# Optimization experiments

Measured on AMD Instinct MI355X. Metric: run time of the kernel, lower is better.

The kernel has to match this reference:

```python
import jax, jax.numpy as jnp
import numpy as np

NF, NLOC, NALL, NNEI = 2, 2048, 3072, 128
Q_DIM = K_DIM = V_DIM = 256
H, D = 8, 32  # num_heads, head_dim
TOTAL = H * D


def setup_inputs() -> dict:
    key = jax.random.key(0)
    ks = jax.random.split(key, 12)
    inp = {
        "q": jax.random.normal(ks[0], (NF, NLOC, Q_DIM), jnp.float32),
        "k": jax.random.normal(ks[1], (NF, NALL, K_DIM), jnp.float32),
        "v": jax.random.normal(ks[2], (NF, NALL, V_DIM), jnp.float32),
        "nlist": jax.random.randint(ks[3], (NF, NLOC, NNEI), 0, NALL, jnp.int64),
        "bias": jax.random.normal(ks[4], (NF, H, NLOC, NNEI), jnp.float32),
        # torch Linear weights: [out, in]
        "Wq": jax.random.normal(ks[5], (TOTAL, Q_DIM), jnp.float32) * 0.05,
        "Wk": jax.random.normal(ks[6], (TOTAL, K_DIM), jnp.float32) * 0.05,
        "Wv": jax.random.normal(ks[7], (TOTAL, V_DIM), jnp.float32) * 0.05,
        "Wg": jax.random.normal(ks[8], (TOTAL, Q_DIM), jnp.float32) * 0.05,
        "bg": jnp.ones((TOTAL,), jnp.float32),  # gating init: bias=1
        "Wo": jax.random.normal(ks[9], (Q_DIM, TOTAL), jnp.float32) * 0.05,
        "bo": jnp.zeros((Q_DIM,), jnp.float32),
    }
    return inp


def reference(q, k, v, nlist, bias, Wq, Wk, Wv, Wg, bg, Wo, bo):
    nf, nloc, _ = q.shape
    nnei = nlist.shape[-1]
    norm = D ** (-0.5)

    g = q @ Wg.T + bg                       # [nf, nloc, TOTAL]
    qh = (q @ Wq.T) * norm                  # [nf, nloc, TOTAL]
    kh = k @ Wk.T                           # [nf, nall, TOTAL]
    vh = v @ Wv.T                           # [nf, nall, TOTAL]

    # gather neighbors: [nf, nloc, nnei, TOTAL]
    fidx = jnp.arange(nf)[:, None, None]
    kg = kh[fidx, nlist].reshape(nf, nloc, nnei, H, D)
    vg = vh[fidx, nlist].reshape(nf, nloc, nnei, H, D)
    qh = qh.reshape(nf, nloc, H, D)

    # per-atom attention: single query vs nnei neighbors
    attn = jnp.einsum("fnhd,fnihd->fhni", qh, kg)      # [nf, H, nloc, nnei]
    attn = jax.nn.softmax(attn + bias, axis=-1)
    o = jnp.einsum("fhni,fnihd->fnhd", attn, vg)       # [nf, nloc, H, D]
    o = o.reshape(nf, nloc, TOTAL)

    o = jax.nn.sigmoid(g) * o
    return o @ Wo.T + bo
```

## Files before the change

kernel.cpp:

```cpp
#include <hip/hip_runtime.h>

#define NF_   2
#define NLOC_ 2048
#define NALL_ 3072
#define NNEI_ 128
#define H_    8
#define D_    32
#define CH_   256

typedef __attribute__((ext_vector_type(8))) short  short8v;
typedef __attribute__((ext_vector_type(8))) unsigned short ushort8v;
typedef __attribute__((ext_vector_type(4))) float  floatx4;

__device__ __forceinline__ unsigned short f2bf(float x) {
  unsigned u = __float_as_uint(x);
  unsigned r = u + 0x7fff + ((u >> 16) & 1);
  return (unsigned short)(r >> 16);
}
__device__ __forceinline__ float bf2f(unsigned short h) {
  return __uint_as_float(((unsigned)h) << 16);
}

__device__ __forceinline__ void cvt_store(unsigned short* hp, unsigned short* lp,
                                          float4 u, float4 v) {
  ushort8v hv, lv;
  hv[0] = f2bf(u.x); lv[0] = f2bf(u.x - bf2f(hv[0]));
  hv[1] = f2bf(u.y); lv[1] = f2bf(u.y - bf2f(hv[1]));
  hv[2] = f2bf(u.z); lv[2] = f2bf(u.z - bf2f(hv[2]));
  hv[3] = f2bf(u.w); lv[3] = f2bf(u.w - bf2f(hv[3]));
  hv[4] = f2bf(v.x); lv[4] = f2bf(v.x - bf2f(hv[4]));
  hv[5] = f2bf(v.y); lv[5] = f2bf(v.y - bf2f(hv[5]));
  hv[6] = f2bf(v.z); lv[6] = f2bf(v.z - bf2f(hv[6]));
  hv[7] = f2bf(v.w); lv[7] = f2bf(v.w - bf2f(hv[7]));
  *(ushort8v*)hp = hv;
  *(ushort8v*)lp = lv;
}

__global__ __launch_bounds__(256) void wcvt_kernel(
    const float* __restrict__ W0, const float* __restrict__ W1,
    const float* __restrict__ W2, const float* __restrict__ W3,
    const float* __restrict__ W4, unsigned short* __restrict__ dst) {
  const float* srcs[5] = {W0, W1, W2, W3, W4};
  const float* s = srcs[blockIdx.y];
  unsigned short* hi = dst + (size_t)blockIdx.y * 2 * 65536;
  unsigned short* lo = hi + 65536;
  const int idx = (blockIdx.x * 256 + threadIdx.x) * 4;
  const float4 v = *(const float4*)(s + idx);
  unsigned short h0 = f2bf(v.x), h1 = f2bf(v.y), h2 = f2bf(v.z), h3 = f2bf(v.w);
  ushort4 hv = {h0, h1, h2, h3};
  ushort4 lv = {f2bf(v.x - bf2f(h0)), f2bf(v.y - bf2f(h1)),
                f2bf(v.z - bf2f(h2)), f2bf(v.w - bf2f(h3))};
  *(ushort4*)(hi + idx) = hv;
  *(ushort4*)(lo + idx) = lv;
}

__device__ __forceinline__ void gemm_mfma(
    const float* __restrict__ A,
    const unsigned short* __restrict__ Whi, const unsigned short* __restrict__ Wlo,
    const float* __restrict__ bvec, float* __restrict__ C,
    int M, int mode,
    unsigned short (*Ah)[40], unsigned short (*Al)[40],
    unsigned short (*Wh)[40], unsigned short (*Wl)[40]) {
  const int t  = threadIdx.x;
  const int m0 = blockIdx.y * 128;
  if (m0 >= M) return;
  const int n0 = blockIdx.x * 64;

  const int lane = t & 63;
  const int wv   = t >> 6;
  const int wr   = wv >> 1;
  const int wc   = wv & 1;
  const int l15  = lane & 15;
  const int ko   = (lane >> 4) * 8;

  const int sr = t >> 1;
  const int sk = (t & 1) * 16;
  const int wrow = t >> 2;
  const int wk   = (t & 3) * 8;

  floatx4 acc[4][2] = {};

  for (int k0 = 0; k0 < 256; k0 += 32) {
    const float* Ap = A + (size_t)(m0 + sr) * 256 + k0 + sk;
    const float4 a0 = *(const float4*)(Ap + 0);
    const float4 a1 = *(const float4*)(Ap + 4);
    const float4 a2 = *(const float4*)(Ap + 8);
    const float4 a3 = *(const float4*)(Ap + 12);
    const size_t woff = (size_t)(n0 + wrow) * 256 + k0 + wk;
    const uint4 whv = *(const uint4*)(Whi + woff);
    const uint4 wlv = *(const uint4*)(Wlo + woff);
    __syncthreads();
    cvt_store(&Ah[sr][sk + 0], &Al[sr][sk + 0], a0, a1);
    cvt_store(&Ah[sr][sk + 8], &Al[sr][sk + 8], a2, a3);
    *(uint4*)&Wh[wrow][wk] = whv;
    *(uint4*)&Wl[wrow][wk] = wlv;
    __syncthreads();

    short8v afh[4], afl[4], bfh[2], bfl[2];
#pragma unroll
    for (int mi = 0; mi < 4; ++mi) {
      const int rr = wr * 64 + mi * 16 + l15;
      afh[mi] = *(const short8v*)&Ah[rr][ko];
      afl[mi] = *(const short8v*)&Al[rr][ko];
    }
#pragma unroll
    for (int ni = 0; ni < 2; ++ni) {
      const int rr = wc * 32 + ni * 16 + l15;
      bfh[ni] = *(const short8v*)&Wh[rr][ko];
      bfl[ni] = *(const short8v*)&Wl[rr][ko];
    }
#pragma unroll
    for (int mi = 0; mi < 4; ++mi)
#pragma unroll
      for (int ni = 0; ni < 2; ++ni) {
        acc[mi][ni] = __builtin_amdgcn_mfma_f32_16x16x32_bf16(
            afh[mi], bfh[ni], acc[mi][ni], 0, 0, 0);
        acc[mi][ni] = __builtin_amdgcn_mfma_f32_16x16x32_bf16(
            afh[mi], bfl[ni], acc[mi][ni], 0, 0, 0);
        acc[mi][ni] = __builtin_amdgcn_mfma_f32_16x16x32_bf16(
            afl[mi], bfh[ni], acc[mi][ni], 0, 0, 0);
      }
  }

  const float norm = 0.17677669529663687f;
#pragma unroll
  for (int mi = 0; mi < 4; ++mi)
#pragma unroll
    for (int ni = 0; ni < 2; ++ni) {
      const int col = n0 + wc * 32 + ni * 16 + l15;
      const float bv = (mode == 1 || mode == 3) ? bvec[col] : 0.f;
#pragma unroll
      for (int r = 0; r < 4; ++r) {
        const int row = m0 + wr * 64 + mi * 16 + (lane >> 4) * 4 + r;
        float vv = acc[mi][ni][r];
        if (mode == 0)      vv *= norm;
        else if (mode == 1) vv = 1.f / (1.f + __expf(-(vv + bv)));
        else if (mode == 3) vv += bv;
        C[(size_t)row * 256 + col] = vv;
      }
    }
}

__global__ __launch_bounds__(256, 3) void proj_kernel(
    const float* __restrict__ q, const float* __restrict__ k, const float* __restrict__ v,
    const unsigned short* __restrict__ whl, const float* __restrict__ bg,
    float* __restrict__ qh, float* __restrict__ gs,
    float* __restrict__ kh, float* __restrict__ vh) {
  __shared__ unsigned short Ah[128][40], Al[128][40], Wh[64][40], Wl[64][40];
  const unsigned short* Whi = whl + (size_t)blockIdx.z * 2 * 65536;
  const unsigned short* Wlo = Whi + 65536;
  switch (blockIdx.z) {
    case 0:  gemm_mfma(q, Whi, Wlo, nullptr, qh, NF_ * NLOC_, 0, Ah, Al, Wh, Wl); break;
    case 1:  gemm_mfma(q, Whi, Wlo, bg,      gs, NF_ * NLOC_, 1, Ah, Al, Wh, Wl); break;
    case 2:  gemm_mfma(k, Whi, Wlo, nullptr, kh, NF_ * NALL_, 2, Ah, Al, Wh, Wl); break;
    default: gemm_mfma(v, Whi, Wlo, nullptr, vh, NF_ * NALL_, 2, Ah, Al, Wh, Wl); break;
  }
}

__global__ __launch_bounds__(256, 3) void out_gemm_kernel(
    const float* __restrict__ x, const unsigned short* __restrict__ whl,
    const float* __restrict__ bo, float* __restrict__ out) {
  __shared__ unsigned short Ah[128][40], Al[128][40], Wh[64][40], Wl[64][40];
  const unsigned short* Whi = whl + (size_t)4 * 2 * 65536;
  const unsigned short* Wlo = Whi + 65536;
  gemm_mfma(x, Whi, Wlo, bo, out, NF_ * NLOC_, 3, Ah, Al, Wh, Wl);
}

__global__ __launch_bounds__(256, 4) void attn_kernel(
    const float* __restrict__ qh, const float* __restrict__ gs,
    const float* __restrict__ kh, const float* __restrict__ vh,
    const void* __restrict__ nlist, const float* __restrict__ bias,
    float* __restrict__ x) {
  __shared__ float q_s[CH_];
  __shared__ int   jn[NNEI_];
  __shared__ float p[H_][NNEI_ + 4];
  __shared__ float K_s[32][256];

  const int t   = threadIdx.x;
  const int bid = blockIdx.x;
  const int f   = bid >> 11;
  const int n   = bid & (NLOC_ - 1);
  const size_t row = (size_t)bid;

  q_s[t] = qh[row * CH_ + t];

  const int* nl32 = (const int*)nlist;
  int odd_or = 0;
#pragma unroll
  for (int w = 1; w < 16; w += 2) odd_or |= nl32[w];
  if (t < NNEI_) {
    if (odd_or == 0) {
      const long long* nl64 = (const long long*)nlist;
      jn[t] = (int)nl64[row * NNEI_ + t];
    } else {
      jn[t] = nl32[row * NNEI_ + t];
    }
  }
  __syncthreads();

  const int h  = t >> 5;
  const int il = t & 31;
  const int w  = t >> 6;
  const int l  = t & 63;

  float4 qv[8];
  {
    const float4* qp = (const float4*)(q_s + h * D_);
#pragma unroll
    for (int i = 0; i < 8; ++i) qv[i] = qp[i];
  }

  const float* kbase = kh + (size_t)f * NALL_ * CH_;
  const float* bb    = bias + (((size_t)f * H_ + h) * NLOC_ + n) * NNEI_;

  float s[4];
#pragma unroll
  for (int c = 0; c < 4; ++c) {
    if (c) __syncthreads();
#pragma unroll
    for (int u = 0; u < 8; ++u) {
      const int r = w * 8 + u;
      const int j = jn[c * 32 + r];
      const float4 kv = *(const float4*)(kbase + (size_t)j * CH_ + l * 4);
      *(float4*)(&K_s[r][(l ^ (r & 7)) * 4]) = kv;
    }
    __syncthreads();
    const int swz = il & 7;
    const float4* krow = (const float4*)(&K_s[il][0]);
    float a = 0.f;
#pragma unroll
    for (int d4 = 0; d4 < 8; ++d4) {
      const float4 kv = krow[(h * 8 + d4) ^ swz];
      a = fmaf(qv[d4].x, kv.x, a);
      a = fmaf(qv[d4].y, kv.y, a);
      a = fmaf(qv[d4].z, kv.z, a);
      a = fmaf(qv[d4].w, kv.w, a);
    }
    s[c] = a + bb[c * 32 + il];
  }

  float m = fmaxf(fmaxf(s[0], s[1]), fmaxf(s[2], s[3]));
#pragma unroll
  for (int off = 16; off >= 1; off >>= 1) m = fmaxf(m, __shfl_xor(m, off));
  float e[4];
  float sum = 0.f;
#pragma unroll
  for (int r = 0; r < 4; ++r) { e[r] = __expf(s[r] - m); sum += e[r]; }
#pragma unroll
  for (int off = 16; off >= 1; off >>= 1) sum += __shfl_xor(sum, off);
  const float inv = 1.f / sum;
#pragma unroll
  for (int r = 0; r < 4; ++r) p[h][il + 32 * r] = e[r] * inv;
  __syncthreads();

  const float* vb = vh + (size_t)f * NALL_ * CH_ + h * D_ + il;
  float ac0 = 0.f, ac1 = 0.f, ac2 = 0.f, ac3 = 0.f;
  for (int i = 0; i < NNEI_; i += 4) {
    const float4 p4 = *(const float4*)(&p[h][i]);
    const int4  j4 = *(const int4*)(&jn[i]);
    ac0 = fmaf(p4.x, vb[(size_t)j4.x * CH_], ac0);
    ac1 = fmaf(p4.y, vb[(size_t)j4.y * CH_], ac1);
    ac2 = fmaf(p4.z, vb[(size_t)j4.z * CH_], ac2);
    ac3 = fmaf(p4.w, vb[(size_t)j4.w * CH_], ac3);
  }
  const float acc = (ac0 + ac1) + (ac2 + ac3);

  const float g = gs[row * CH_ + t];
  x[row * CH_ + t] = g * acc;
}

extern "C" void kernel_launch(void* const* d_in, const int* in_sizes, int n_in,
                              void* d_out, int out_size, void* d_ws, size_t ws_size,
                              hipStream_t stream) {
  const float* q     = (const float*)d_in[0];
  const float* k     = (const float*)d_in[1];
  const float* v     = (const float*)d_in[2];
  const void*  nlist = d_in[3];
  const float* bias  = (const float*)d_in[4];
  const float* Wq    = (const float*)d_in[5];
  const float* Wk    = (const float*)d_in[6];
  const float* Wv    = (const float*)d_in[7];
  const float* Wg    = (const float*)d_in[8];
  const float* bg    = (const float*)d_in[9];
  const float* Wo    = (const float*)d_in[10];
  const float* bo    = (const float*)d_in[11];
  float* out = (float*)d_out;

  float* ws = (float*)d_ws;
  float* qh = ws;
  float* gs = qh + (size_t)NF_ * NLOC_ * CH_;
  float* kh = gs + (size_t)NF_ * NLOC_ * CH_;
  float* vh = kh + (size_t)NF_ * NALL_ * CH_;
  float* x  = vh + (size_t)NF_ * NALL_ * CH_;
  unsigned short* whl = (unsigned short*)(x + (size_t)NF_ * NLOC_ * CH_);

  wcvt_kernel<<<dim3(64, 5), 256, 0, stream>>>(Wq, Wg, Wk, Wv, Wo, whl);
  proj_kernel<<<dim3(4, 48, 4), 256, 0, stream>>>(q, k, v, whl, bg,
                                                  qh, gs, kh, vh);
  attn_kernel<<<dim3(NF_ * NLOC_), 256, 0, stream>>>(qh, gs, kh, vh, nlist, bias, x);
  out_gemm_kernel<<<dim3(4, 32), 256, 0, stream>>>(x, whl, bo, out);
}
```

Measured before the change: 185.3 us.

## Pre-split activations to bf16 hi/lo and vectorize attention PV gather

Adds a separate conversion pass that splits q/k/v into bf16 hi/lo arrays once, so the projection GEMM tiles only copy pre-split data instead of converting fp32 in every block (q was converted twice, once for the Wq and once for the Wg projection). The attention kernel now writes its output directly as bf16 hi/lo, which removes the conversion from the output GEMM. The PV accumulation is restructured so each wave takes a quarter of the neighbors and loads float4 vectors of V, with a cross-wave reduction in shared memory. The cost is an extra kernel launch and extra global traffic for the hi/lo activation copies.

```diff
diff --git a/kernel.cpp b/kernel.cpp
--- a/kernel.cpp
+++ b/kernel.cpp
@@ -19,21 +19,6 @@
 }
 __device__ __forceinline__ float bf2f(unsigned short h) {
   return __uint_as_float(((unsigned)h) << 16);
-}
-
-__device__ __forceinline__ void cvt_store(unsigned short* hp, unsigned short* lp,
-                                          float4 u, float4 v) {
-  ushort8v hv, lv;
-  hv[0] = f2bf(u.x); lv[0] = f2bf(u.x - bf2f(hv[0]));
-  hv[1] = f2bf(u.y); lv[1] = f2bf(u.y - bf2f(hv[1]));
-  hv[2] = f2bf(u.z); lv[2] = f2bf(u.z - bf2f(hv[2]));
-  hv[3] = f2bf(u.w); lv[3] = f2bf(u.w - bf2f(hv[3]));
-  hv[4] = f2bf(v.x); lv[4] = f2bf(v.x - bf2f(hv[4]));
-  hv[5] = f2bf(v.y); lv[5] = f2bf(v.y - bf2f(hv[5]));
-  hv[6] = f2bf(v.z); lv[6] = f2bf(v.z - bf2f(hv[6]));
-  hv[7] = f2bf(v.w); lv[7] = f2bf(v.w - bf2f(hv[7]));
-  *(ushort8v*)hp = hv;
-  *(ushort8v*)lp = lv;
 }
 
 __global__ __launch_bounds__(256) void wcvt_kernel(
@@ -54,8 +39,33 @@
   *(ushort4*)(lo + idx) = lv;
 }
 
+#define QN_ ((size_t)NF_ * NLOC_ * CH_)
+#define KN_ ((size_t)NF_ * NALL_ * CH_)
+
+__global__ __launch_bounds__(256) void acvt_kernel(
+    const float* __restrict__ q, const float* __restrict__ k,
+    const float* __restrict__ v, unsigned short* __restrict__ dst) {
+  const int m = blockIdx.y;
+  const float* src;
+  unsigned short* hi;
+  size_t n;
+  if (m == 0)      { src = q; hi = dst;                 n = QN_; }
+  else if (m == 1) { src = k; hi = dst + 2 * QN_;       n = KN_; }
+  else             { src = v; hi = dst + 2 * QN_ + 2 * KN_; n = KN_; }
+  unsigned short* lo = hi + n;
+  const size_t idx = ((size_t)blockIdx.x * 256 + threadIdx.x) * 4;
+  if (idx >= n) return;
+  const float4 val = *(const float4*)(src + idx);
+  unsigned short h0 = f2bf(val.x), h1 = f2bf(val.y), h2 = f2bf(val.z), h3 = f2bf(val.w);
+  ushort4 hv = {h0, h1, h2, h3};
+  ushort4 lv = {f2bf(val.x - bf2f(h0)), f2bf(val.y - bf2f(h1)),
+                f2bf(val.z - bf2f(h2)), f2bf(val.w - bf2f(h3))};
+  *(ushort4*)(hi + idx) = hv;
+  *(ushort4*)(lo + idx) = lv;
+}
+
 __device__ __forceinline__ void gemm_mfma(
-    const float* __restrict__ A,
+    const unsigned short* __restrict__ Ahi, const unsigned short* __restrict__ Alo,
     const unsigned short* __restrict__ Whi, const unsigned short* __restrict__ Wlo,
     const float* __restrict__ bvec, float* __restrict__ C,
     int M, int mode,
@@ -81,19 +91,22 @@
   floatx4 acc[4][2] = {};
 
   for (int k0 = 0; k0 < 256; k0 += 32) {
-    const float* Ap = A + (size_t)(m0 + sr) * 256 + k0 + sk;
-    const float4 a0 = *(const float4*)(Ap + 0);
-    const float4 a1 = *(const float4*)(Ap + 4);
-    const float4 a2 = *(const float4*)(Ap + 8);
-    const float4 a3 = *(const float4*)(Ap + 12);
+    const unsigned short* Aph = Ahi + (size_t)(m0 + sr) * 256 + k0 + sk;
+    const unsigned short* Apl = Alo + (size_t)(m0 + sr) * 256 + k0 + sk;
+    const ushort8v ah0 = *(const ushort8v*)(Aph);
+    const ushort8v ah1 = *(const ushort8v*)(Aph + 8);
+    const ushort8v al0 = *(const ushort8v*)(Apl);
+    const ushort8v al1 = *(const ushort8v*)(Apl + 8);
     const size_t woff = (size_t)(n0 + wrow) * 256 + k0 + wk;
-    const uint4 whv = *(const uint4*)(Whi + woff);
-    const uint4 wlv = *(const uint4*)(Wlo + woff);
+    const ushort8v whv = *(const ushort8v*)(Whi + woff);
+    const ushort8v wlv = *(const ushort8v*)(Wlo + woff);
     __syncthreads();
-    cvt_store(&Ah[sr][sk + 0], &Al[sr][sk + 0], a0, a1);
-    cvt_store(&Ah[sr][sk + 8], &Al[sr][sk + 8], a2, a3);
-    *(uint4*)&Wh[wrow][wk] = whv;
-    *(uint4*)&Wl[wrow][wk] = wlv;
+    *(ushort8v*)&Ah[sr][sk + 0] = ah0;
+    *(ushort8v*)&Ah[sr][sk + 8] = ah1;
+    *(ushort8v*)&Al[sr][sk + 0] = al0;
+    *(ushort8v*)&Al[sr][sk + 8] = al1;
+    *(ushort8v*)&Wh[wrow][wk] = whv;
+    *(ushort8v*)&Wl[wrow][wk] = wlv;
     __syncthreads();
 
     short8v afh[4], afl[4], bfh[2], bfl[2];
@@ -142,35 +155,38 @@
 }
 
 __global__ __launch_bounds__(256, 3) void proj_kernel(
-    const float* __restrict__ q, const float* __restrict__ k, const float* __restrict__ v,
-    const unsigned short* __restrict__ whl, const float* __restrict__ bg,
+    const unsigned short* __restrict__ ahl, const unsigned short* __restrict__ whl,
+    const float* __restrict__ bg,
     float* __restrict__ qh, float* __restrict__ gs,
     float* __restrict__ kh, float* __restrict__ vh) {
   __shared__ unsigned short Ah[128][40], Al[128][40], Wh[64][40], Wl[64][40];
   const unsigned short* Whi = whl + (size_t)blockIdx.z * 2 * 65536;
   const unsigned short* Wlo = Whi + 65536;
+  const unsigned short* qhi = ahl;
+  const unsigned short* khi = ahl + 2 * QN_;
+  const unsigned short* vhi = ahl + 2 * QN_ + 2 * KN_;
   switch (blockIdx.z) {
-    case 0:  gemm_mfma(q, Whi, Wlo, nullptr, qh, NF_ * NLOC_, 0, Ah, Al, Wh, Wl); break;
-    case 1:  gemm_mfma(q, Whi, Wlo, bg,      gs, NF_ * NLOC_, 1, Ah, Al, Wh, Wl); break;
-    case 2:  gemm_mfma(k, Whi, Wlo, nullptr, kh, NF_ * NALL_, 2, Ah, Al, Wh, Wl); break;
-    default: gemm_mfma(v, Whi, Wlo, nullptr, vh, NF_ * NALL_, 2, Ah, Al, Wh, Wl); break;
+    case 0:  gemm_mfma(qhi, qhi + QN_, Whi, Wlo, nullptr, qh, NF_ * NLOC_, 0, Ah, Al, Wh, Wl); break;
+    case 1:  gemm_mfma(qhi, qhi + QN_, Whi, Wlo, bg,      gs, NF_ * NLOC_, 1, Ah, Al, Wh, Wl); break;
+    case 2:  gemm_mfma(khi, khi + KN_, Whi, Wlo, nullptr, kh, NF_ * NALL_, 2, Ah, Al, Wh, Wl); break;
+    default: gemm_mfma(vhi, vhi + KN_, Whi, Wlo, nullptr, vh, NF_ * NALL_, 2, Ah, Al, Wh, Wl); break;
   }
 }
 
 __global__ __launch_bounds__(256, 3) void out_gemm_kernel(
-    const float* __restrict__ x, const unsigned short* __restrict__ whl,
+    const unsigned short* __restrict__ xhl, const unsigned short* __restrict__ whl,
     const float* __restrict__ bo, float* __restrict__ out) {
   __shared__ unsigned short Ah[128][40], Al[128][40], Wh[64][40], Wl[64][40];
   const unsigned short* Whi = whl + (size_t)4 * 2 * 65536;
   const unsigned short* Wlo = Whi + 65536;
-  gemm_mfma(x, Whi, Wlo, bo, out, NF_ * NLOC_, 3, Ah, Al, Wh, Wl);
+  gemm_mfma(xhl, xhl + QN_, Whi, Wlo, bo, out, NF_ * NLOC_, 3, Ah, Al, Wh, Wl);
 }
 
 __global__ __launch_bounds__(256, 4) void attn_kernel(
     const float* __restrict__ qh, const float* __restrict__ gs,
     const float* __restrict__ kh, const float* __restrict__ vh,
     const void* __restrict__ nlist, const float* __restrict__ bias,
-    float* __restrict__ x) {
+    unsigned short* __restrict__ xhi, unsigned short* __restrict__ xlo) {
   __shared__ float q_s[CH_];
   __shared__ int   jn[NNEI_];
   __shared__ float p[H_][NNEI_ + 4];
@@ -253,20 +269,46 @@
   for (int r = 0; r < 4; ++r) p[h][il + 32 * r] = e[r] * inv;
   __syncthreads();
 
-  const float* vb = vh + (size_t)f * NALL_ * CH_ + h * D_ + il;
-  float ac0 = 0.f, ac1 = 0.f, ac2 = 0.f, ac3 = 0.f;
-  for (int i = 0; i < NNEI_; i += 4) {
-    const float4 p4 = *(const float4*)(&p[h][i]);
-    const int4  j4 = *(const int4*)(&jn[i]);
-    ac0 = fmaf(p4.x, vb[(size_t)j4.x * CH_], ac0);
-    ac1 = fmaf(p4.y, vb[(size_t)j4.y * CH_], ac1);
-    ac2 = fmaf(p4.z, vb[(size_t)j4.z * CH_], ac2);
-    ac3 = fmaf(p4.w, vb[(size_t)j4.w * CH_], ac3);
-  }
-  const float acc = (ac0 + ac1) + (ac2 + ac3);
-
-  const float g = gs[row * CH_ + t];
-  x[row * CH_ + t] = g * acc;
+  float* red = (float*)K_s;
+  {
+    const int g  = w;
+    const int h2 = l >> 3;
+    const int d4 = l & 7;
+    float4 pv4[8];
+#pragma unroll
+    for (int jj = 0; jj < 8; ++jj)
+      pv4[jj] = *(const float4*)(&p[h2][g * 32 + jj * 4]);
+    const float* vb2 = vh + (size_t)f * NALL_ * CH_ + h2 * D_ + d4 * 4;
+    float4 a4 = {0.f, 0.f, 0.f, 0.f};
+#pragma unroll
+    for (int jj = 0; jj < 8; ++jj) {
+      const int j0 = jn[g * 32 + jj * 4 + 0];
+      const int j1 = jn[g * 32 + jj * 4 + 1];
+      const int j2 = jn[g * 32 + jj * 4 + 2];
+      const int j3 = jn[g * 32 + jj * 4 + 3];
+      const float4 v0 = *(const float4*)(vb2 + (size_t)j0 * CH_);
+      const float4 v1 = *(const float4*)(vb2 + (size_t)j1 * CH_);
+      const float4 v2 = *(const float4*)(vb2 + (size_t)j2 * CH_);
+      const float4 v3 = *(const float4*)(vb2 + (size_t)j3 * CH_);
+      a4.x = fmaf(pv4[jj].x, v0.x, a4.x); a4.y = fmaf(pv4[jj].x, v0.y, a4.y);
+      a4.z = fmaf(pv4[jj].x, v0.z, a4.z); a4.w = fmaf(pv4[jj].x, v0.w, a4.w);
+      a4.x = fmaf(pv4[jj].y, v1.x, a4.x); a4.y = fmaf(pv4[jj].y, v1.y, a4.y);
+      a4.z = fmaf(pv4[jj].y, v1.z, a4.z); a4.w = fmaf(pv4[jj].y, v1.w, a4.w);
+      a4.x = fmaf(pv4[jj].z, v2.x, a4.x); a4.y = fmaf(pv4[jj].z, v2.y, a4.y);
+      a4.z = fmaf(pv4[jj].z, v2.z, a4.z); a4.w = fmaf(pv4[jj].z, v2.w, a4.w);
+      a4.x = fmaf(pv4[jj].w, v3.x, a4.x); a4.y = fmaf(pv4[jj].w, v3.y, a4.y);
+      a4.z = fmaf(pv4[jj].w, v3.z, a4.z); a4.w = fmaf(pv4[jj].w, v3.w, a4.w);
+    }
+    *(float4*)(&red[g * 256 + h2 * 32 + d4 * 4]) = a4;
+  }
+  __syncthreads();
+
+  const float gt = gs[row * CH_ + t];
+  const float o = (red[t] + red[256 + t]) + (red[512 + t] + red[768 + t]);
+  const float xo = gt * o;
+  const unsigned short hh = f2bf(xo);
+  xhi[row * CH_ + t] = hh;
+  xlo[row * CH_ + t] = f2bf(xo - bf2f(hh));
 }
 
 extern "C" void kernel_launch(void* const* d_in, const int* in_sizes, int n_in,
@@ -288,15 +330,17 @@
 
   float* ws = (float*)d_ws;
   float* qh = ws;
-  float* gs = qh + (size_t)NF_ * NLOC_ * CH_;
-  float* kh = gs + (size_t)NF_ * NLOC_ * CH_;
-  float* vh = kh + (size_t)NF_ * NALL_ * CH_;
-  float* x  = vh + (size_t)NF_ * NALL_ * CH_;
-  unsigned short* whl = (unsigned short*)(x + (size_t)NF_ * NLOC_ * CH_);
+  float* gs = qh + QN_;
+  float* kh = gs + QN_;
+  float* vh = kh + KN_;
+  unsigned short* xhl = (unsigned short*)(vh + KN_);
+  unsigned short* whl = xhl + 2 * QN_;
+  unsigned short* ahl = whl + 5 * 2 * 65536;
 
   wcvt_kernel<<<dim3(64, 5), 256, 0, stream>>>(Wq, Wg, Wk, Wv, Wo, whl);
-  proj_kernel<<<dim3(4, 48, 4), 256, 0, stream>>>(q, k, v, whl, bg,
-                                                  qh, gs, kh, vh);
-  attn_kernel<<<dim3(NF_ * NLOC_), 256, 0, stream>>>(qh, gs, kh, vh, nlist, bias, x);
-  out_gemm_kernel<<<dim3(4, 32), 256, 0, stream>>>(x, whl, bo, out);
-}
+  acvt_kernel<<<dim3(1536, 3), 256, 0, stream>>>(q, k, v, ahl);
+  proj_kernel<<<dim3(4, 48, 4), 256, 0, stream>>>(ahl, whl, bg, qh, gs, kh, vh);
+  attn_kernel<<<dim3(NF_ * NLOC_), 256, 0, stream>>>(qh, gs, kh, vh, nlist, bias,
+                                                     xhl, xhl + QN_);
+  out_gemm_kernel<<<dim3(4, 32), 256, 0, stream>>>(xhl, whl, bo, out);
+}
```

Result: slower. 243.1 us (+31.2%).
